# Performance work log

Hardware: AMD Instinct MI355X
Metric: run time of the kernel (lower is better)

The kernel has to match this reference:

```python
import jax, jax.numpy as jnp
import numpy as np

N_ATOMS = 100_000
N_PAIRS = 6_400_000
N_BATCH = 16


def smooth_switch(x, x0, x1):
    t = (x - x0) / (x1 - x0)
    tc = jnp.clip(t, 1e-9, 1.0 - 1e-9)  # safe interior values
    f1 = jnp.exp(-1.0 / tc)
    f2 = jnp.exp(-1.0 / (1.0 - tc))
    s = f1 / (f1 + f2)
    return jnp.where(t <= 0.0, 0.0, jnp.where(t >= 1.0, 1.0, s))


def setup_inputs() -> dict:
    key = jax.random.key(0)
    k1, k2, k3, k4, k5 = jax.random.split(key, 5)
    atomic_numbers = jax.random.randint(k1, (N_ATOMS,), 1, 81).astype(jnp.float32)
    # displacements scaled so distances span the (0, 10) switch window
    displacements = jax.random.normal(k2, (N_PAIRS, 3), dtype=jnp.float32) * 2.5
    idx_i = jnp.sort(jax.random.randint(k3, (N_PAIRS,), 0, N_ATOMS)).astype(jnp.int32)
    idx_j = jax.random.randint(k4, (N_PAIRS,), 0, N_ATOMS).astype(jnp.int32)
    atom_mask = jnp.ones((N_ATOMS,), dtype=jnp.float32)
    batch_mask = jnp.ones((N_PAIRS,), dtype=jnp.float32)
    batch_segments = jnp.sort(jax.random.randint(k5, (N_ATOMS,), 0, N_BATCH)).astype(jnp.int32)
    # ZBL parameters (non-trainable constants in the module)
    a_coefficient = jnp.asarray(0.8854, dtype=jnp.float32)
    a_exponent = jnp.asarray(0.23, dtype=jnp.float32)
    phi_coefficients = jnp.asarray([0.18175, 0.50986, 0.28022, 0.02817], dtype=jnp.float32)
    phi_exponents = jnp.asarray([3.1998, 0.94229, 0.4029, 0.20162], dtype=jnp.float32)
    return {
        "atomic_numbers": atomic_numbers,
        "displacements": displacements,
        "idx_i": idx_i,
        "idx_j": idx_j,
        "atom_mask": atom_mask,
        "batch_mask": batch_mask,
        "batch_segments": batch_segments,
        "batch_size": N_BATCH,
        "a_coefficient": a_coefficient,
        "a_exponent": a_exponent,
        "phi_coefficients": phi_coefficients,
        "phi_exponents": phi_exponents,
    }


def reference(atomic_numbers, displacements, idx_i, idx_j, atom_mask, batch_mask,
              batch_segments, batch_size, a_coefficient, a_exponent,
              phi_coefficients, phi_exponents):
    n_atoms = atomic_numbers.shape[0]
    displacements = displacements + (1.0 - batch_mask[..., None])
    distances = jnp.maximum(jnp.linalg.norm(displacements, axis=-1), 1e-10)  # [P]
    switch_off = smooth_switch(distances, 0.0, 10.0)

    safe_atomic_numbers = jnp.maximum(atomic_numbers, 1e-06)
    za = jnp.exp(jnp.log(safe_atomic_numbers) * jnp.abs(a_exponent))
    za = jnp.nan_to_num(za, nan=1e-06, posinf=1e6, neginf=1e-06)
    za_sum = za[idx_i] + za[idx_j]                     # [P]
    denominator = jnp.maximum(za_sum, 1e-06)
    a_ij = jnp.abs(a_coefficient) / denominator
    a_ij = jnp.nan_to_num(a_ij, nan=1e-06, posinf=1e6, neginf=1e-06)
    arguments = jnp.maximum(distances, 1e-10) / jnp.maximum(a_ij, 1e-10)
    arguments = jnp.nan_to_num(arguments, nan=1e-06, posinf=1e6, neginf=1e-06)

    raw_coefficients = jnp.abs(phi_coefficients)
    coefficients = raw_coefficients / jnp.maximum(jnp.sum(raw_coefficients), 1e-10)
    exponents = jnp.maximum(jnp.abs(phi_exponents), 1e-10)
    log_terms = -exponents[None, :] * arguments[:, None]          # [P,4]
    max_log = jnp.max(log_terms, axis=1, keepdims=True)           # [P,1]
    exp_terms = jnp.exp(log_terms - max_log)
    exp_terms = jnp.nan_to_num(exp_terms, nan=0.0, posinf=1.0, neginf=0.0)
    phi = jnp.sum(coefficients[None, :] * exp_terms, axis=1) * jnp.exp(max_log)[..., 0]
    phi = jnp.maximum(phi, 1e-30)
    phi = jnp.nan_to_num(phi, nan=1e-30, posinf=1e6, neginf=1e-30)

    safe_distances = jnp.maximum(distances, 1e-10)
    safe_phi = jnp.maximum(phi, 1e-30)
    safe_switch = jnp.maximum(switch_off, 1e-30)
    charge_product = jnp.minimum(safe_atomic_numbers[idx_i] * safe_atomic_numbers[idx_j], 1e4)
    base_repulsion = jnp.minimum(0.5 * charge_product / safe_distances, 1e6)
    repulsion = base_repulsion * safe_phi * safe_switch
    repulsion = jnp.clip(repulsion, 0.0, 1e6)
    repulsion = jnp.nan_to_num(repulsion, nan=0.0, posinf=1e6, neginf=0.0)
    repulsion = repulsion * batch_mask

    Erep = jax.ops.segment_sum(repulsion, segment_ids=idx_i, num_segments=n_atoms)
    Erep = Erep * atom_mask
    Erep = jnp.clip(Erep, 0.0, 1e6)
    Erep = jnp.nan_to_num(Erep, nan=0.0, posinf=1e6, neginf=0.0)
    Erep = Erep * 0.01
    return Erep[..., None, None, None]  # [N,1,1,1]
```

## Files before the change

### kernel.cpp

```cpp
#include <hip/hip_runtime.h>
#include <math.h>


#define LOG2E 1.4426950408889634f
#define BLK   1024
#define NBLK  256
#define PPT   4
#define STRD  (BLK * PPT)
#define CAP   2048

static __device__ __forceinline__ float rcpf_(float x)  { return __builtin_amdgcn_rcpf(x); }
static __device__ __forceinline__ float rsqf_(float x)  { return __builtin_amdgcn_rsqf(x); }
static __device__ __forceinline__ float exp2f_(float x) { return __builtin_amdgcn_exp2f(x); }
static __device__ __forceinline__ float log2f_(float x) { return __builtin_amdgcn_logf(x); }

struct G4 { int ii0,ii1,ii2,ii3, jj0,jj1,jj2,jj3;
            float bm0,bm1,bm2,bm3;
            float dx0,dx1,dx2,dx3, dy0,dy1,dy2,dy3, dz0,dz1,dz2,dz3; };

__global__ void zbl_k0(const float* __restrict__ an,
                       unsigned char* __restrict__ z8,
                       float* __restrict__ out, int n) {
    int i = blockIdx.x * blockDim.x + threadIdx.x;
    if (i >= n) return;
    int z = (int)(an[i] + 0.5f);
    z8[i] = (unsigned char)min(max(z, 1), 255);
    out[i] = 0.0f;
}

static __device__ __forceinline__ G4 loadG4(const int* __restrict__ idx_i,
                                            const int* __restrict__ idx_j,
                                            const float* __restrict__ bmk,
                                            const float* __restrict__ disp,
                                            int p0, int cend) {
    G4 g;
    if (p0 + PPT <= cend) {
        const int4   ii = *reinterpret_cast<const int4*>(idx_i + p0);
        const int4   jj = *reinterpret_cast<const int4*>(idx_j + p0);
        const float4 bm = *reinterpret_cast<const float4*>(bmk + p0);
        const float4* d4 = reinterpret_cast<const float4*>(disp + (long)p0 * 3);
        const float4 d0 = d4[0], d1 = d4[1], d2 = d4[2];
        g.ii0=ii.x; g.ii1=ii.y; g.ii2=ii.z; g.ii3=ii.w;
        g.jj0=jj.x; g.jj1=jj.y; g.jj2=jj.z; g.jj3=jj.w;
        g.bm0=bm.x; g.bm1=bm.y; g.bm2=bm.z; g.bm3=bm.w;
        g.dx0=d0.x; g.dy0=d0.y; g.dz0=d0.z;
        g.dx1=d0.w; g.dy1=d1.x; g.dz1=d1.y;
        g.dx2=d1.z; g.dy2=d1.w; g.dz2=d2.x;
        g.dx3=d2.y; g.dy3=d2.z; g.dz3=d2.w;
    } else {
        int   ii[4], jj[4]; float bm[4], dx[4], dy[4], dz[4];
        #pragma unroll
        for (int k = 0; k < PPT; ++k) {
            const int p = p0 + k;
            if (p < cend) {
                ii[k] = idx_i[p]; jj[k] = idx_j[p]; bm[k] = bmk[p];
                const float* dp = disp + (long)p * 3;
                dx[k] = dp[0]; dy[k] = dp[1]; dz[k] = dp[2];
            } else { ii[k] = -1; jj[k] = 0; bm[k] = 0.f; dx[k]=dy[k]=dz[k]=0.f; }
        }
        g.ii0=ii[0]; g.ii1=ii[1]; g.ii2=ii[2]; g.ii3=ii[3];
        g.jj0=jj[0]; g.jj1=jj[1]; g.jj2=jj[2]; g.jj3=jj[3];
        g.bm0=bm[0]; g.bm1=bm[1]; g.bm2=bm[2]; g.bm3=bm[3];
        g.dx0=dx[0]; g.dx1=dx[1]; g.dx2=dx[2]; g.dx3=dx[3];
        g.dy0=dy[0]; g.dy1=dy[1]; g.dy2=dy[2]; g.dy3=dy[3];
        g.dz0=dz[0]; g.dz1=dz[1]; g.dz2=dz[2]; g.dz3=dz[3];
    }
    return g;
}

__global__ __launch_bounds__(BLK) void zbl_pair_kernel(
    const float* __restrict__ disp,
    const int*   __restrict__ idx_i,
    const int*   __restrict__ idx_j,
    const float* __restrict__ batch_mask,
    const unsigned char* __restrict__ z8g,
    const float* __restrict__ a_coef_ptr,
    const float* __restrict__ a_exp_ptr,
    const float* __restrict__ phi_c,
    const float* __restrict__ phi_e,
    float* __restrict__ out_acc,
    int nA, int nP)
{
    extern __shared__ unsigned char smem[];
    const int nA_pad = (nA + 15) & ~15;
    unsigned char* s_z8  = smem;
    float*         s_za  = (float*)(smem + nA_pad);
    float*         s_acc = (float*)(smem + nA_pad + 1024);

    const int tid = threadIdx.x;

    {
        const int nw = nA >> 4;
        const uint4* g4 = reinterpret_cast<const uint4*>(z8g);
        uint4* s4 = reinterpret_cast<uint4*>(s_z8);
        for (int i = tid; i < nw; i += BLK) s4[i] = g4[i];
        for (int i = (nw << 4) + tid; i < nA; i += BLK) s_z8[i] = z8g[i];
    }
    if (tid < 256) {
        float ae = fabsf(a_exp_ptr[0]);
        int z = max(tid, 1);
        s_za[tid] = exp2f_(ae * log2f_((float)z));
    }
    for (int i = tid; i < CAP; i += BLK) s_acc[i] = 0.0f;

    const float ac_inv = rcpf_(fmaxf(fabsf(a_coef_ptr[0]), 1e-10f));
    float c0 = fabsf(phi_c[0]), c1 = fabsf(phi_c[1]);
    float c2 = fabsf(phi_c[2]), c3 = fabsf(phi_c[3]);
    const float cinv = rcpf_(fmaxf(c0 + c1 + c2 + c3, 1e-10f));
    c0 *= cinv; c1 *= cinv; c2 *= cinv; c3 *= cinv;
    const float e0 = fmaxf(fabsf(phi_e[0]), 1e-10f);
    const float e1 = fmaxf(fabsf(phi_e[1]), 1e-10f);
    const float e2 = fmaxf(fabsf(phi_e[2]), 1e-10f);
    const float e3 = fmaxf(fabsf(phi_e[3]), 1e-10f);

    int chunk = (nP + NBLK - 1) / NBLK;
    chunk = (chunk + PPT - 1) & ~(PPT - 1);
    const int cbeg = min(blockIdx.x * chunk, nP);
    const int cend = min(cbeg + chunk, nP);
    const int lane = tid & 63;
    const int kbase = (cbeg < nP) ? idx_i[cbeg] : 0;

    __syncthreads();

#define PAIR_REP(II, JJ, BM, DX, DY, DZ, rep)                                   \
    {                                                                           \
        rep = 0.0f;                                                             \
        if ((II) >= 0) {                                                        \
            const int zi = (int)s_z8[(II)];                                     \
            const int zj = (int)s_z8[(JJ)];                                     \
            const float za_i = s_za[zi];                                        \
            const float za_j = s_za[zj];                                        \
            const float add = 1.0f - (BM);                                      \
            const float dx = (DX) + add, dy = (DY) + add, dz = (DZ) + add;      \
            float d2   = fmaxf(dx * dx + dy * dy + dz * dz, 1e-20f);            \
            float rsq  = rsqf_(d2);                                             \
            float dist = d2 * rsq;                                              \
            float tt = dist * 0.1f;                                             \
            float tc = fminf(fmaxf(tt, 1e-9f), 1.0f - 1e-9f);                   \
            float u  = (1.0f - 2.0f * tc) * rcpf_(tc - tc * tc);                \
            float s  = rcpf_(1.0f + exp2f_(u * LOG2E));                         \
            float sw = (tt >= 1.0f) ? 1.0f : s;                                 \
            float za_sum = za_i + za_j;                                         \
            float arg  = fminf(dist * za_sum * ac_inv, 1e6f);                   \
            float narg = -arg * LOG2E;                                          \
            float phi  = c0 * exp2f_(e0 * narg) + c1 * exp2f_(e1 * narg) +      \
                         c2 * exp2f_(e2 * narg) + c3 * exp2f_(e3 * narg);       \
            phi = fminf(fmaxf(phi, 1e-30f), 1e6f);                              \
            float cp   = fminf((float)(zi * zj), 1e4f);                         \
            float brep = fminf(0.5f * cp * rsq, 1e6f);                          \
            float r    = brep * phi * fmaxf(sw, 1e-30f);                        \
            r = fminf(fmaxf(r, 0.0f), 1e6f);                                    \
            if (!(r == r)) r = 0.0f;                                            \
            rep = r * (BM);                                                     \
        }                                                                       \
    }

#define DEPOSIT(k, v)                                                           \
    {                                                                           \
        if ((k) >= 0) {                                                         \
            int slot = (k) - kbase;                                             \
            if (slot < CAP) atomicAdd(&s_acc[slot], (v));                       \
            else            atomicAdd(&out_acc[k], (v));                        \
        }                                                                       \
    }

#define MERGE(K, R)                                                             \
    {                                                                           \
        if ((K) == runkey) runsum += (R);                                       \
        else { DEPOSIT(runkey, runsum); runkey = (K); runsum = (R); }           \
    }

    G4 s0 = loadG4(idx_i, idx_j, batch_mask, disp, cbeg + tid * PPT,            cend);
    G4 s1 = loadG4(idx_i, idx_j, batch_mask, disp, cbeg + STRD + tid * PPT,     cend);

    for (int pb = cbeg; pb < cend; pb += STRD) {
        G4 s2 = loadG4(idx_i, idx_j, batch_mask, disp,
                       pb + 2 * STRD + tid * PPT, cend);

        float r0, r1, r2, r3;
        PAIR_REP(s0.ii0, s0.jj0, s0.bm0, s0.dx0, s0.dy0, s0.dz0, r0);
        PAIR_REP(s0.ii1, s0.jj1, s0.bm1, s0.dx1, s0.dy1, s0.dz1, r1);
        PAIR_REP(s0.ii2, s0.jj2, s0.bm2, s0.dx2, s0.dy2, s0.dz2, r2);
        PAIR_REP(s0.ii3, s0.jj3, s0.bm3, s0.dx3, s0.dy3, s0.dz3, r3);

        int   runkey = s0.ii0;
        float runsum = r0;
        MERGE(s0.ii1, r1);
        MERGE(s0.ii2, r2);
        MERGE(s0.ii3, r3);

        {
            const int k0_ = __shfl(runkey, 0);
            if (__all(runkey == k0_)) {
                float v = runsum;
                #pragma unroll
                for (int d = 1; d < 64; d <<= 1) v += __shfl_xor(v, d);
                if (lane == 0) DEPOSIT(k0_, v);
            } else {
                float v = runsum;
                int   k = runkey;
                #pragma unroll
                for (int d = 1; d < 64; d <<= 1) {
                    float nv = __shfl_down(v, d);
                    int   nk = __shfl_down(k, d);
                    if (lane + d < 64 && nk == k) v += nv;
                }
                int pk = __shfl_up(k, 1);
                bool head = (lane == 0) || (pk != k);
                if (head) DEPOSIT(k, v);
            }
        }

        s0 = s1; s1 = s2;
    }
#undef PAIR_REP
#undef DEPOSIT
#undef MERGE

    __syncthreads();
    for (int s = tid; s < CAP; s += BLK) {
        float v = s_acc[s];
        int   k = kbase + s;
        if (v != 0.0f && k < nA) atomicAdd(&out_acc[k], v);
    }
}

__global__ void zbl_epilogue(float* __restrict__ out,
                             const float* __restrict__ atom_mask, int n) {
    int i = blockIdx.x * blockDim.x + threadIdx.x;
    if (i >= n) return;
    float v = out[i] * atom_mask[i];
    v = fminf(fmaxf(v, 0.0f), 1e6f);
    if (!(v == v)) v = 0.0f;
    out[i] = v * 0.01f;
}

extern "C" void kernel_launch(void* const* d_in, const int* in_sizes, int n_in,
                              void* d_out, int out_size, void* d_ws, size_t ws_size,
                              hipStream_t stream) {
    const float* an         = (const float*)d_in[0];
    const float* disp       = (const float*)d_in[1];
    const int*   idx_i      = (const int*)d_in[2];
    const int*   idx_j      = (const int*)d_in[3];
    const float* atom_mask  = (const float*)d_in[4];
    const float* batch_mask = (const float*)d_in[5];
    const float* a_coef     = (const float*)d_in[8];
    const float* a_exp      = (const float*)d_in[9];
    const float* phi_c      = (const float*)d_in[10];
    const float* phi_e      = (const float*)d_in[11];

    const int nA = in_sizes[0];
    const int nP = in_sizes[2];
    float* out = (float*)d_out;

    unsigned char* z8 = (unsigned char*)d_ws;

    zbl_k0<<<(nA + 255) / 256, 256, 0, stream>>>(an, z8, out, nA);

    const int nA_pad = (nA + 15) & ~15;
    const size_t smem = (size_t)nA_pad + 1024 + (size_t)CAP * sizeof(float);
    zbl_pair_kernel<<<NBLK, BLK, smem, stream>>>(
        disp, idx_i, idx_j, batch_mask, z8, a_coef, a_exp, phi_c, phi_e,
        out, nA, nP);

    zbl_epilogue<<<(nA + 255) / 256, 256, 0, stream>>>(out, atom_mask, nA);
}
```

Measured before the change: 44.86 us.

## Prefetch atomic numbers one stage ahead, inline Z^a, and defer the wave scan by one iteration

Moves the shared-memory atomic-number lookups for the next pair tile ahead of the current tile's math, so LDS latency overlaps with computation. Replaces the Z^a lookup table with inline log2/exp2 evaluation, which removes the second dependent LDS load and frees the table's shared memory. The segmented wave reduction now runs on the previous iteration's partial sums, and the uniform-key fast path is dropped, leaving the full segmented scan on every iteration. The trade is more transcendental work per pair and more live registers in exchange for shorter dependency chains.

Measured after the change: 46.12 us. 1.03x slower.

```diff
diff --git a/kernel.cpp b/kernel.cpp
--- a/kernel.cpp
+++ b/kernel.cpp
@@ -84,8 +84,7 @@
     extern __shared__ unsigned char smem[];
     const int nA_pad = (nA + 15) & ~15;
     unsigned char* s_z8  = smem;
-    float*         s_za  = (float*)(smem + nA_pad);
-    float*         s_acc = (float*)(smem + nA_pad + 1024);
+    float*         s_acc = (float*)(smem + nA_pad);
 
     const int tid = threadIdx.x;
 
@@ -96,13 +95,9 @@
         for (int i = tid; i < nw; i += BLK) s4[i] = g4[i];
         for (int i = (nw << 4) + tid; i < nA; i += BLK) s_z8[i] = z8g[i];
     }
-    if (tid < 256) {
-        float ae = fabsf(a_exp_ptr[0]);
-        int z = max(tid, 1);
-        s_za[tid] = exp2f_(ae * log2f_((float)z));
-    }
     for (int i = tid; i < CAP; i += BLK) s_acc[i] = 0.0f;
 
+    const float ae     = fabsf(a_exp_ptr[0]);
     const float ac_inv = rcpf_(fmaxf(fabsf(a_coef_ptr[0]), 1e-10f));
     float c0 = fabsf(phi_c[0]), c1 = fabsf(phi_c[1]);
     float c2 = fabsf(phi_c[2]), c3 = fabsf(phi_c[3]);
@@ -122,14 +117,14 @@
 
     __syncthreads();
 
-#define PAIR_REP(II, JJ, BM, DX, DY, DZ, rep)                                   \
+#define PAIR_REP(II, JJ, ZI, ZJ, BM, DX, DY, DZ, rep)                           \
     {                                                                           \
         rep = 0.0f;                                                             \
         if ((II) >= 0) {                                                        \
-            const int zi = (int)s_z8[(II)];                                     \
-            const int zj = (int)s_z8[(JJ)];                                     \
-            const float za_i = s_za[zi];                                        \
-            const float za_j = s_za[zj];                                        \
+            const float zif = (float)(ZI);                                      \
+            const float zjf = (float)(ZJ);                                      \
+            const float za_i = exp2f_(ae * log2f_(zif));                        \
+            const float za_j = exp2f_(ae * log2f_(zjf));                        \
             const float add = 1.0f - (BM);                                      \
             const float dx = (DX) + add, dy = (DY) + add, dz = (DZ) + add;      \
             float d2   = fmaxf(dx * dx + dy * dy + dz * dz, 1e-20f);            \
@@ -146,7 +141,7 @@
             float phi  = c0 * exp2f_(e0 * narg) + c1 * exp2f_(e1 * narg) +      \
                          c2 * exp2f_(e2 * narg) + c3 * exp2f_(e3 * narg);       \
             phi = fminf(fmaxf(phi, 1e-30f), 1e6f);                              \
-            float cp   = fminf((float)(zi * zj), 1e4f);                         \
+            float cp   = fminf(zif * zjf, 1e4f);                                \
             float brep = fminf(0.5f * cp * rsq, 1e6f);                          \
             float r    = brep * phi * fmaxf(sw, 1e-30f);                        \
             r = fminf(fmaxf(r, 0.0f), 1e6f);                                    \
@@ -170,18 +165,45 @@
         else { DEPOSIT(runkey, runsum); runkey = (K); runsum = (R); }           \
     }
 
-    G4 s0 = loadG4(idx_i, idx_j, batch_mask, disp, cbeg + tid * PPT,            cend);
-    G4 s1 = loadG4(idx_i, idx_j, batch_mask, disp, cbeg + STRD + tid * PPT,     cend);
+#define SCAN_DEPOSIT(PK, PS)                                                    \
+    {                                                                           \
+        float v = (PS);                                                         \
+        int   k = (PK);                                                         \
+        _Pragma("unroll")                                                       \
+        for (int d = 1; d < 64; d <<= 1) {                                      \
+            float nv = __shfl_down(v, d);                                       \
+            int   nk = __shfl_down(k, d);                                       \
+            if (lane + d < 64 && nk == k) v += nv;                              \
+        }                                                                       \
+        int pk2 = __shfl_up(k, 1);                                              \
+        bool head = (lane == 0) || (pk2 != k);                                  \
+        if (head) DEPOSIT(k, v);                                                \
+    }
+
+    G4 s0 = loadG4(idx_i, idx_j, batch_mask, disp, cbeg + tid * PPT,        cend);
+    G4 s1 = loadG4(idx_i, idx_j, batch_mask, disp, cbeg + STRD + tid * PPT, cend);
+    int czi0 = (int)s_z8[max(s0.ii0, 0)], czj0 = (int)s_z8[s0.jj0];
+    int czi1 = (int)s_z8[max(s0.ii1, 0)], czj1 = (int)s_z8[s0.jj1];
+    int czi2 = (int)s_z8[max(s0.ii2, 0)], czj2 = (int)s_z8[s0.jj2];
+    int czi3 = (int)s_z8[max(s0.ii3, 0)], czj3 = (int)s_z8[s0.jj3];
+
+    int   pkey = -1;
+    float psum = 0.0f;
 
     for (int pb = cbeg; pb < cend; pb += STRD) {
         G4 s2 = loadG4(idx_i, idx_j, batch_mask, disp,
                        pb + 2 * STRD + tid * PPT, cend);
 
+        int nzi0 = (int)s_z8[max(s1.ii0, 0)], nzj0 = (int)s_z8[s1.jj0];
+        int nzi1 = (int)s_z8[max(s1.ii1, 0)], nzj1 = (int)s_z8[s1.jj1];
+        int nzi2 = (int)s_z8[max(s1.ii2, 0)], nzj2 = (int)s_z8[s1.jj2];
+        int nzi3 = (int)s_z8[max(s1.ii3, 0)], nzj3 = (int)s_z8[s1.jj3];
+
         float r0, r1, r2, r3;
-        PAIR_REP(s0.ii0, s0.jj0, s0.bm0, s0.dx0, s0.dy0, s0.dz0, r0);
-        PAIR_REP(s0.ii1, s0.jj1, s0.bm1, s0.dx1, s0.dy1, s0.dz1, r1);
-        PAIR_REP(s0.ii2, s0.jj2, s0.bm2, s0.dx2, s0.dy2, s0.dz2, r2);
-        PAIR_REP(s0.ii3, s0.jj3, s0.bm3, s0.dx3, s0.dy3, s0.dz3, r3);
+        PAIR_REP(s0.ii0, s0.jj0, czi0, czj0, s0.bm0, s0.dx0, s0.dy0, s0.dz0, r0);
+        PAIR_REP(s0.ii1, s0.jj1, czi1, czj1, s0.bm1, s0.dx1, s0.dy1, s0.dz1, r1);
+        PAIR_REP(s0.ii2, s0.jj2, czi2, czj2, s0.bm2, s0.dx2, s0.dy2, s0.dz2, r2);
+        PAIR_REP(s0.ii3, s0.jj3, czi3, czj3, s0.bm3, s0.dx3, s0.dy3, s0.dz3, r3);
 
         int   runkey = s0.ii0;
         float runsum = r0;
@@ -189,33 +211,20 @@
         MERGE(s0.ii2, r2);
         MERGE(s0.ii3, r3);
 
-        {
-            const int k0_ = __shfl(runkey, 0);
-            if (__all(runkey == k0_)) {
-                float v = runsum;
-                #pragma unroll
-                for (int d = 1; d < 64; d <<= 1) v += __shfl_xor(v, d);
-                if (lane == 0) DEPOSIT(k0_, v);
-            } else {
-                float v = runsum;
-                int   k = runkey;
-                #pragma unroll
-                for (int d = 1; d < 64; d <<= 1) {
-                    float nv = __shfl_down(v, d);
-                    int   nk = __shfl_down(k, d);
-                    if (lane + d < 64 && nk == k) v += nv;
-                }
-                int pk = __shfl_up(k, 1);
-                bool head = (lane == 0) || (pk != k);
-                if (head) DEPOSIT(k, v);
-            }
-        }
+        SCAN_DEPOSIT(pkey, psum);
 
         s0 = s1; s1 = s2;
-    }
+        czi0 = nzi0; czj0 = nzj0; czi1 = nzi1; czj1 = nzj1;
+        czi2 = nzi2; czj2 = nzj2; czi3 = nzi3; czj3 = nzj3;
+        pkey = runkey; psum = runsum;
+    }
+
+    SCAN_DEPOSIT(pkey, psum);
+
 #undef PAIR_REP
 #undef DEPOSIT
 #undef MERGE
+#undef SCAN_DEPOSIT
 
     __syncthreads();
     for (int s = tid; s < CAP; s += BLK) {
@@ -258,7 +267,7 @@
     zbl_k0<<<(nA + 255) / 256, 256, 0, stream>>>(an, z8, out, nA);
 
     const int nA_pad = (nA + 15) & ~15;
-    const size_t smem = (size_t)nA_pad + 1024 + (size_t)CAP * sizeof(float);
+    const size_t smem = (size_t)nA_pad + (size_t)CAP * sizeof(float);
     zbl_pair_kernel<<<NBLK, BLK, smem, stream>>>(
         disp, idx_i, idx_j, batch_mask, z8, a_coef, a_exp, phi_c, phi_e,
         out, nA, nP);
```
